# Kernel tuning notes

Measured on AMD Instinct MI355X. Metric: run time of the kernel, lower is better.

The kernel has to match this reference:

```python
import jax, jax.numpy as jnp
import numpy as np

N_POP = 10000.0   # total population N
DT = 0.01         # integration step
EPS = 1e-6        # clamp floor, matches torch .clamp(min=1e-06)
B = 32768         # number of Monte-Carlo trajectories
NUM_STEPS = 1000  # int(T / dt) with T=10, dt=0.01


def setup_inputs() -> dict:
    key = jax.random.key(0)
    k_dw, = jax.random.split(key, 1)
    beta = jnp.array([0.3], dtype=jnp.float32)
    sigma = jnp.array([0.2], dtype=jnp.float32)
    gamma = jnp.array([0.1], dtype=jnp.float32)
    S0 = jnp.full((B,), 9990.0, dtype=jnp.float32)
    E0 = jnp.zeros((B,), dtype=jnp.float32)
    I0 = jnp.full((B,), 10.0, dtype=jnp.float32)
    R0 = jnp.zeros((B,), dtype=jnp.float32)
    # Brownian increments before sqrt(dt) scaling; shared across batch as in the
    # original (torch.randn(4, 1) per step regardless of batch size).
    dW = jax.random.normal(k_dw, (NUM_STEPS, 4), dtype=jnp.float32)
    return {"beta": beta, "sigma": sigma, "gamma": gamma,
            "S0": S0, "E0": E0, "I0": I0, "R0": R0, "dW": dW}


def reference(beta, sigma, gamma, S0, E0, I0, R0, dW):
    b, sg, gm = beta[0], sigma[0], gamma[0]
    dWs = dW * jnp.sqrt(jnp.float32(DT))  # [num_steps, 4], scaled increments

    def step(carry, dw):
        S, E, I, R = carry
        S = jnp.maximum(S, EPS)
        E = jnp.maximum(E, EPS)
        I = jnp.maximum(I, EPS)
        R = jnp.maximum(R, EPS)
        inf_rate = b * S * I / N_POP          # beta*S*I/N
        exp_rate = sg * E                     # sigma*E
        rec_rate = gm * I                     # gamma*I
        # drift
        dS = -inf_rate * DT
        dE = (inf_rate - exp_rate) * DT
        dI = (exp_rate - rec_rate) * DT
        dR = rec_rate * DT
        # diffusion (g @ dW with the sparse structure of g_S..g_R)
        n_inf = jnp.sqrt(inf_rate)
        n_exp = jnp.sqrt(exp_rate)
        n_rec = jnp.sqrt(rec_rate)
        S_n = S + dS - n_inf * dw[0]
        E_n = E + dE + n_inf * dw[0] - n_exp * dw[1]
        I_n = I + dI + n_exp * dw[1] - n_rec * dw[2]
        R_n = R + dR + n_rec * dw[2]
        return (S_n, E_n, I_n, R_n), jnp.stack([S_n, E_n, I_n, R_n])  # [4, B]

    _, traj = jax.lax.scan(step, (S0, E0, I0, R0), dWs)
    return traj  # [num_steps, 4, B]: S/E/I/R trajectories
```

## Files before the change

kernel.cpp:

```cpp
#include <hip/hip_runtime.h>


constexpr int   B_TRAJ  = 32768;
constexpr int   NSTEPS  = 1000;
constexpr int   K       = 20;
constexpr int   NC      = NSTEPS / K;
constexpr float DT      = 0.01f;
constexpr float EPS     = 1e-6f;
constexpr float INV_N   = 1.0f / 10000.0f;

__device__ __forceinline__ void barrier_lds_only() {
    asm volatile("s_waitcnt lgkmcnt(0)" ::: "memory");
    __builtin_amdgcn_s_barrier();
    asm volatile("" ::: "memory");
}

__global__ __launch_bounds__(128) void seir_sde_kernel(
    const float* __restrict__ beta,
    const float* __restrict__ sigma,
    const float* __restrict__ gamma,
    const float* __restrict__ S0,
    const float* __restrict__ E0,
    const float* __restrict__ I0,
    const float* __restrict__ R0,
    const float4* __restrict__ dW,
    float* __restrict__ out)
{
    __shared__ float4 wbuf[NSTEPS];
    __shared__ float  ring[2][K][4][64];

    const float btnD = beta[0] * INV_N * DT;
    const float sgD  = sigma[0] * DT;
    const float gmD  = gamma[0] * DT;
    const float sbi  = __builtin_amdgcn_sqrtf(btnD);
    const float sbe  = __builtin_amdgcn_sqrtf(sgD);
    const float sbr  = __builtin_amdgcn_sqrtf(gmD);

    for (int i = threadIdx.x; i < NSTEPS; i += 128) {
        const float4 w = dW[i];
        wbuf[i] = make_float4(w.x * sbi, w.y * sbe, w.z * sbr, 0.0f);
    }

    const int lane = threadIdx.x & 63;
    const int wid  = threadIdx.x >> 6;

    float S=0.f, E=0.f, I=0.f, R=0.f;
    if (wid == 0) {
        const int b = blockIdx.x * 64 + lane;
        S = S0[b]; E = E0[b]; I = I0[b]; R = R0[b];
    }

    float* const obase = out + blockIdx.x * 64
                             + (lane >> 4) * B_TRAJ + (lane & 15) * 4;

    #define SEIR_STEP(w, dst)                                                  \
    {                                                                          \
        const float Sc = fmaxf(S, EPS);                                        \
        const float Ec = fmaxf(E, EPS);                                        \
        const float Ic = fmaxf(I, EPS);                                        \
        const float Rc = fmaxf(R, EPS);                                        \
        const float P  = Sc * Ic;                                              \
        const float iD = btnD * P;                                             \
        const float eD = sgD * Ec;                                             \
        const float rD = gmD * Ic;                                             \
        const float ai = __builtin_amdgcn_sqrtf(P)  * (w).x;                   \
        const float ae = __builtin_amdgcn_sqrtf(Ec) * (w).y;                   \
        const float ar = __builtin_amdgcn_sqrtf(Ic) * (w).z;                   \
        const float Sn = Sc - iD - ai;                                         \
        const float En = Ec + iD - eD + ai - ae;                               \
        const float In = Ic + eD - rD + ae - ar;                               \
        const float Rn = Rc + rD + ar;                                         \
        (dst)[0][lane] = Sn;                                                   \
        (dst)[1][lane] = En;                                                   \
        (dst)[2][lane] = In;                                                   \
        (dst)[3][lane] = Rn;                                                   \
        S = Sn; E = En; I = In; R = Rn;                                        \
    }

    #define FILL(c)                                                            \
    {                                                                          \
        const int s0 = (c) * K;                                                \
        float (*rw)[4][64] = ring[(c) & 1];                                    \
        _Pragma("unroll")                                                      \
        for (int k = 0; k < K; ++k) {                                          \
            const float4 w = wbuf[s0 + k];                                     \
            SEIR_STEP(w, rw[k]);                                               \
        }                                                                      \
    }

    #define STORE_CHUNK(c, v)                                                  \
    {                                                                          \
        const float4* rd = (const float4*)&ring[(c) & 1][0][0][0];             \
        float* o = obase + (size_t)((c) * K) * (4 * B_TRAJ);                   \
        _Pragma("unroll")                                                      \
        for (int k = 0; k < K; ++k) v[k] = rd[k * 64 + lane];                  \
        _Pragma("unroll")                                                      \
        for (int k = 0; k < K; ++k) {                                          \
            *(float4*)o = v[k];                                                \
            o += 4 * B_TRAJ;                                                   \
        }                                                                      \
    }

    float4 va[K], vb[K];

    __syncthreads();

    if (wid == 0) FILL(0);
    barrier_lds_only();

    for (int cc = 0; cc < NC; cc += 2) {
        if (wid == 0) { FILL(cc + 1); }
        else          { STORE_CHUNK(cc, va); }
        barrier_lds_only();
        if (wid == 0) { if (cc + 2 < NC) FILL(cc + 2); }
        else          { STORE_CHUNK(cc + 1, vb); }
        barrier_lds_only();
    }
    #undef SEIR_STEP
    #undef FILL
    #undef STORE_CHUNK
}

extern "C" void kernel_launch(void* const* d_in, const int* in_sizes, int n_in,
                              void* d_out, int out_size, void* d_ws, size_t ws_size,
                              hipStream_t stream) {
    const float*  beta  = (const float*)d_in[0];
    const float*  sigma = (const float*)d_in[1];
    const float*  gamma = (const float*)d_in[2];
    const float*  S0    = (const float*)d_in[3];
    const float*  E0    = (const float*)d_in[4];
    const float*  I0    = (const float*)d_in[5];
    const float*  R0    = (const float*)d_in[6];
    const float4* dW    = (const float4*)d_in[7];
    float* out = (float*)d_out;

    seir_sde_kernel<<<B_TRAJ / 64, 128, 0, stream>>>(
        beta, sigma, gamma, S0, E0, I0, R0, dW, out);
}
```

Baseline: 94.17 us.

## Compute two trajectories per lane and use two store wavefronts per block

The compute wavefront now advances two independent trajectories per lane, with paired float2 LDS writes. Each block now covers 128 trajectories, served by two storer wavefronts that each write two of the four compartments. This exposes instruction-level parallelism in the serial recurrence and halves the number of blocks. The cost is fewer blocks for occupancy, more registers per lane, and a larger LDS ring.

```diff
diff --git a/kernel.cpp b/kernel.cpp
--- a/kernel.cpp
+++ b/kernel.cpp
@@ -5,6 +5,7 @@
 constexpr int   NSTEPS  = 1000;
 constexpr int   K       = 20;
 constexpr int   NC      = NSTEPS / K;
+constexpr int   TPB     = 128;
 constexpr float DT      = 0.01f;
 constexpr float EPS     = 1e-6f;
 constexpr float INV_N   = 1.0f / 10000.0f;
@@ -15,7 +16,7 @@
     asm volatile("" ::: "memory");
 }
 
-__global__ __launch_bounds__(128) void seir_sde_kernel(
+__global__ __launch_bounds__(192) void seir_sde_kernel(
     const float* __restrict__ beta,
     const float* __restrict__ sigma,
     const float* __restrict__ gamma,
@@ -27,7 +28,7 @@
     float* __restrict__ out)
 {
     __shared__ float4 wbuf[NSTEPS];
-    __shared__ float  ring[2][K][4][64];
+    __shared__ float  ring[2][K][4][TPB];
 
     const float btnD = beta[0] * INV_N * DT;
     const float sgD  = sigma[0] * DT;
@@ -36,7 +37,7 @@
     const float sbe  = __builtin_amdgcn_sqrtf(sgD);
     const float sbr  = __builtin_amdgcn_sqrtf(gmD);
 
-    for (int i = threadIdx.x; i < NSTEPS; i += 128) {
+    for (int i = threadIdx.x; i < NSTEPS; i += 192) {
         const float4 w = dW[i];
         wbuf[i] = make_float4(w.x * sbi, w.y * sbe, w.z * sbr, 0.0f);
     }
@@ -44,56 +45,65 @@
     const int lane = threadIdx.x & 63;
     const int wid  = threadIdx.x >> 6;
 
-    float S=0.f, E=0.f, I=0.f, R=0.f;
+    float Sa=0.f,Ea=0.f,Ia=0.f,Ra=0.f, Sb=0.f,Eb=0.f,Ib=0.f,Rb=0.f;
     if (wid == 0) {
-        const int b = blockIdx.x * 64 + lane;
-        S = S0[b]; E = E0[b]; I = I0[b]; R = R0[b];
+        const int a = blockIdx.x * TPB + 2 * lane;
+        const float2 s2 = *(const float2*)&S0[a];
+        const float2 e2 = *(const float2*)&E0[a];
+        const float2 i2 = *(const float2*)&I0[a];
+        const float2 r2 = *(const float2*)&R0[a];
+        Sa = s2.x; Sb = s2.y; Ea = e2.x; Eb = e2.y;
+        Ia = i2.x; Ib = i2.y; Ra = r2.x; Rb = r2.y;
     }
 
-    float* const obase = out + blockIdx.x * 64
-                             + (lane >> 4) * B_TRAJ + (lane & 15) * 4;
+    const int c0 = (wid - 1) * 2;
+    float* const obase = out + blockIdx.x * TPB
+                             + (c0 + (lane >> 5)) * B_TRAJ + (lane & 31) * 4;
 
-    #define SEIR_STEP(w, dst)                                                  \
+    #define SEIR2(w, dst)                                                      \
     {                                                                          \
-        const float Sc = fmaxf(S, EPS);                                        \
-        const float Ec = fmaxf(E, EPS);                                        \
-        const float Ic = fmaxf(I, EPS);                                        \
-        const float Rc = fmaxf(R, EPS);                                        \
-        const float P  = Sc * Ic;                                              \
-        const float iD = btnD * P;                                             \
-        const float eD = sgD * Ec;                                             \
-        const float rD = gmD * Ic;                                             \
-        const float ai = __builtin_amdgcn_sqrtf(P)  * (w).x;                   \
-        const float ae = __builtin_amdgcn_sqrtf(Ec) * (w).y;                   \
-        const float ar = __builtin_amdgcn_sqrtf(Ic) * (w).z;                   \
-        const float Sn = Sc - iD - ai;                                         \
-        const float En = Ec + iD - eD + ai - ae;                               \
-        const float In = Ic + eD - rD + ae - ar;                               \
-        const float Rn = Rc + rD + ar;                                         \
-        (dst)[0][lane] = Sn;                                                   \
-        (dst)[1][lane] = En;                                                   \
-        (dst)[2][lane] = In;                                                   \
-        (dst)[3][lane] = Rn;                                                   \
-        S = Sn; E = En; I = In; R = Rn;                                        \
+        const float Sc0=fmaxf(Sa,EPS), Ec0=fmaxf(Ea,EPS);                      \
+        const float Ic0=fmaxf(Ia,EPS), Rc0=fmaxf(Ra,EPS);                      \
+        const float Sc1=fmaxf(Sb,EPS), Ec1=fmaxf(Eb,EPS);                      \
+        const float Ic1=fmaxf(Ib,EPS), Rc1=fmaxf(Rb,EPS);                      \
+        const float P0=Sc0*Ic0, P1=Sc1*Ic1;                                    \
+        const float iD0=btnD*P0, eD0=sgD*Ec0, rD0=gmD*Ic0;                     \
+        const float iD1=btnD*P1, eD1=sgD*Ec1, rD1=gmD*Ic1;                     \
+        const float ai0=__builtin_amdgcn_sqrtf(P0) *(w).x;                     \
+        const float ae0=__builtin_amdgcn_sqrtf(Ec0)*(w).y;                     \
+        const float ar0=__builtin_amdgcn_sqrtf(Ic0)*(w).z;                     \
+        const float ai1=__builtin_amdgcn_sqrtf(P1) *(w).x;                     \
+        const float ae1=__builtin_amdgcn_sqrtf(Ec1)*(w).y;                     \
+        const float ar1=__builtin_amdgcn_sqrtf(Ic1)*(w).z;                     \
+        const float Sn0=Sc0-iD0-ai0,  En0=Ec0+iD0-eD0+ai0-ae0;                 \
+        const float In0=Ic0+eD0-rD0+ae0-ar0, Rn0=Rc0+rD0+ar0;                  \
+        const float Sn1=Sc1-iD1-ai1,  En1=Ec1+iD1-eD1+ai1-ae1;                 \
+        const float In1=Ic1+eD1-rD1+ae1-ar1, Rn1=Rc1+rD1+ar1;                  \
+        *(float2*)&(dst)[0][2*lane] = make_float2(Sn0, Sn1);                   \
+        *(float2*)&(dst)[1][2*lane] = make_float2(En0, En1);                   \
+        *(float2*)&(dst)[2][2*lane] = make_float2(In0, In1);                   \
+        *(float2*)&(dst)[3][2*lane] = make_float2(Rn0, Rn1);                   \
+        Sa=Sn0; Ea=En0; Ia=In0; Ra=Rn0;                                        \
+        Sb=Sn1; Eb=En1; Ib=In1; Rb=Rn1;                                        \
     }
 
     #define FILL(c)                                                            \
     {                                                                          \
         const int s0 = (c) * K;                                                \
-        float (*rw)[4][64] = ring[(c) & 1];                                    \
+        float (*rw)[4][TPB] = ring[(c) & 1];                                   \
         _Pragma("unroll")                                                      \
         for (int k = 0; k < K; ++k) {                                          \
             const float4 w = wbuf[s0 + k];                                     \
-            SEIR_STEP(w, rw[k]);                                               \
+            SEIR2(w, rw[k]);                                                   \
         }                                                                      \
     }
 
     #define STORE_CHUNK(c, v)                                                  \
     {                                                                          \
-        const float4* rd = (const float4*)&ring[(c) & 1][0][0][0];             \
+        const float4* rd = (const float4*)&ring[(c) & 1][0][c0][0];            \
         float* o = obase + (size_t)((c) * K) * (4 * B_TRAJ);                   \
         _Pragma("unroll")                                                      \
-        for (int k = 0; k < K; ++k) v[k] = rd[k * 64 + lane];                  \
+        for (int k = 0; k < K; ++k) v[k] = rd[k * (4 * TPB / 4) + lane];       \
         _Pragma("unroll")                                                      \
         for (int k = 0; k < K; ++k) {                                          \
             *(float4*)o = v[k];                                                \
@@ -116,7 +126,7 @@
         else          { STORE_CHUNK(cc + 1, vb); }
         barrier_lds_only();
     }
-    #undef SEIR_STEP
+    #undef SEIR2
     #undef FILL
     #undef STORE_CHUNK
 }
@@ -134,6 +144,6 @@
     const float4* dW    = (const float4*)d_in[7];
     float* out = (float*)d_out;
 
-    seir_sde_kernel<<<B_TRAJ / 64, 128, 0, stream>>>(
+    seir_sde_kernel<<<B_TRAJ / TPB, 192, 0, stream>>>(
         beta, sigma, gamma, S0, E0, I0, R0, dW, out);
 }
```

New measurement: 112.0 us. +18.9%, slower.
